# Kernel tuning notes

Measured on AMD Instinct MI355X. Metric: run time of the kernel, lower is better.

## Reference

```python
import jax, jax.numpy as jnp
import numpy as np

N_QUBITS = 12
N_LAYERS = 2
PATCH = 16
NPS = 14  # patches per side for 224/16
N_PATCHES = NPS * NPS
SCALE = 1.0 / np.sqrt(N_QUBITS)


def _butterfly_gates(n):
    # Faithful replication of QuantumOrthogonalLayer.butterfly_circuit indexing:
    # param_idx increments even when the (idx1, idx2) pair is skipped.
    gates, pidx = [], 0
    n_bl = int(np.ceil(np.log2(n)))
    for layer in range(n_bl):
        stride = 2 ** layer
        for start in range(0, n - stride, 2 * stride):
            for off in range(stride):
                i1, i2 = start + off, start + off + stride
                if i1 < n and i2 < n:
                    gates.append((pidx, i1, i2))
                pidx += 1
    nppl = sum(2 ** (n_bl - 1 - i) * 2 ** i for i in range(n_bl))  # n_params() = 32
    return gates, nppl

GATES, NPPL = _butterfly_gates(N_QUBITS)

# Pauli-Z sign table: qubit 0 is the most-significant bit of the flattened state index.
_bits = (np.arange(2 ** N_QUBITS)[:, None] >> np.arange(N_QUBITS - 1, -1, -1)[None, :]) & 1
Z_SIGNS = jnp.asarray(1.0 - 2.0 * _bits, dtype=jnp.float32)  # (4096, 12)


def _rbs_u(theta):
    # 4x4 real unitary of RY(2t,w1); CNOT(w1,w2); RY(-2t,w1); CNOT(w1,w2)
    c, s = jnp.cos(theta), jnp.sin(theta)
    c2, s2, cs = c * c, s * s, c * s
    return jnp.stack([
        jnp.stack([c2, s2, -cs, cs]),
        jnp.stack([s2, c2, cs, -cs]),
        jnp.stack([cs, -cs, c2, s2]),
        jnp.stack([-cs, cs, s2, c2]),
    ])


def _apply_2q(state, U, i, j):
    # state: (P, 2, 2, ..., 2); apply U to qubit axes i, j
    st = jnp.moveaxis(state, (1 + i, 1 + j), (-2, -1))
    shp = st.shape
    st = st.reshape(shp[:-2] + (4,)) @ U.T
    return jnp.moveaxis(st.reshape(shp), (-2, -1), (1 + i, 1 + j))


@jax.checkpoint
def quantum_expvals(features, params):
    # features: (P, n_qubits) angles; params: (N_LAYERS * NPPL,)
    P = features.shape[0]
    half = 0.5 * features
    amp = jnp.stack([jnp.cos(half), jnp.sin(half)], axis=-1)  # (P, n, 2) RY(x)|0>
    state = jnp.ones((P, 1), features.dtype)
    for q in range(N_QUBITS):  # product-state angle encoding
        state = (state[:, :, None] * amp[:, q][:, None, :]).reshape(P, -1)
    state = state.reshape((P,) + (2,) * N_QUBITS)
    for l in range(N_LAYERS):
        base = l * NPPL
        for pidx, w1, w2 in GATES:
            state = _apply_2q(state, _rbs_u(params[base + pidx]), w1, w2)
    probs = state.reshape(P, -1) ** 2
    return probs @ Z_SIGNS  # (P, n_qubits) <Z_i>


def setup_inputs() -> dict:
    key = jax.random.key(0)
    ks = jax.random.split(key, 6)
    x = jax.random.normal(ks[0], (4, 3, 224, 224), dtype=jnp.float32)
    W_proj = jax.random.normal(ks[1], (N_QUBITS, PATCH * PATCH), dtype=jnp.float32) / np.sqrt(PATCH * PATCH)
    b_proj = jnp.zeros((N_QUBITS,), jnp.float32)
    q_params = 0.1 * jax.random.normal(ks[2], (N_LAYERS * NPPL,), dtype=jnp.float32)
    k_params = 0.1 * jax.random.normal(ks[3], (N_LAYERS * NPPL,), dtype=jnp.float32)
    v_params = 0.1 * jax.random.normal(ks[4], (N_LAYERS * NPPL,), dtype=jnp.float32)
    W_cls = jax.random.normal(ks[5], (1000, N_PATCHES * N_QUBITS), dtype=jnp.float32) / np.sqrt(N_PATCHES * N_QUBITS)
    b_cls = jnp.zeros((1000,), jnp.float32)
    return {"x": x, "W_proj": W_proj, "b_proj": b_proj, "q_params": q_params,
            "k_params": k_params, "v_params": v_params, "W_cls": W_cls, "b_cls": b_cls}


def reference(x, W_proj, b_proj, q_params, k_params, v_params, W_cls, b_cls):
    B = x.shape[0]
    xg = jnp.mean(x, axis=1)  # channel average -> (B, H, W)
    patches = xg.reshape(B, NPS, PATCH, NPS, PATCH).transpose(0, 1, 3, 2, 4)
    patches = patches.reshape(B, N_PATCHES, PATCH * PATCH)
    proj = patches @ W_proj.T + b_proj  # (B, n_patches, n_qubits)
    feats = proj.reshape(-1, N_QUBITS)
    Q = quantum_expvals(feats, q_params).reshape(B, N_PATCHES, N_QUBITS)
    K = quantum_expvals(feats, k_params).reshape(B, N_PATCHES, N_QUBITS)
    V = quantum_expvals(feats, v_params).reshape(B, N_PATCHES, N_QUBITS)
    attn = jax.nn.softmax(jnp.einsum('bqd,bkd->bqk', Q, K) * SCALE, axis=-1)
    out = jnp.einsum('bqk,bkd->bqd', attn, V)  # (B, n_patches, n_qubits)
    logits = out.reshape(B, -1) @ W_cls.T + b_cls
    return logits
```

## Files before the change

### kernel.cpp

```cpp
#include <hip/hip_runtime.h>
#include <math.h>

#define NQ        12
#define NPS       14
#define NPATCH    196
#define NB        4
#define NCLS      1000
#define FEATDIM   2352
#define SCALE_F   0.28867513459481287f

typedef float v2f __attribute__((ext_vector_type(2)));

constexpr int PRa[8][5] = {
    {2,3,0,1, 4},
    {2,3,4,5, 6},
    {2,3,5,6, 7},
    {2,3,0,4, 6},
    {2,3,8,9,10},
    {2,3,9,10,11},
    {2,3,0,8,10},
    {2,3,1,5, 9},
};
constexpr int PTa[8][7] = {
    {5,6,7,8,9,10,11},
    {7,0,1,8,9,10,11},
    {0,1,4,8,9,10,11},
    {8,9,10,1,5,7,11},
    {4,0,1,5,6,7,11},
    {0,1,8,5,6,7,4},
    {1,5,9,6,7,11,4},
    {6,0,11,7,8,10,4},
};
constexpr bool BARa[8] = {false,false,false,false,true,false,false,true};

constexpr int STRIDE = 20;

constexpr int cwgt2(int X, int q) {
    for (int k = 0; k < 4; ++k) if (PRa[X][k] == q) return 1 << k;
    if (PRa[X][4] == q) return 0;
    for (int m = 0; m < 7; ++m) if (PTa[X][m] == q) return STRIDE << m;
    return 0;
}
constexpr int rimm2(int X, int Y, int a) {
    int s = 0;
    for (int j = 0; j < 3; ++j)
        if ((a >> j) & 1) s += cwgt2(X, PRa[Y][2 + j]);
    return s;
}
constexpr int splitpos(int X) {
    int Y = (X + 1) & 7, H = PRa[X][4];
    for (int j = 0; j < 3; ++j) if (PRa[Y][2 + j] == H) return j;
    for (int m = 0; m < 7; ++m) if (PTa[Y][m] == H) return 8 + m;
    return -1;
}

template<int TI>
__device__ __forceinline__ void relayout2(v2f amp2[16], float* lds, int tid, int base) {
    constexpr int X = TI, Y = (TI + 1) & 7;
    constexpr int SP = splitpos(TI);
    constexpr bool BAR = BARa[TI];
    float4* dst = (float4*)(lds + STRIDE * tid);

    #pragma unroll
    for (int k = 0; k < 4; ++k)
        dst[k] = make_float4(amp2[2*k][0], amp2[2*k][1], amp2[2*k+1][0], amp2[2*k+1][1]);
    if (BAR) __syncthreads();

    float4 rvh[4];

    if constexpr (SP < 3) {
        #pragma unroll
        for (int a = 0; a < 8; ++a) {
            if ((a >> SP) & 1) continue;
            float4 v = *(const float4*)(lds + base + rimm2(X, Y, a));
            if (a < 4) {
                amp2[2*a][0]   = v.x; amp2[2*a][1]   = v.y;
                amp2[2*a+1][0] = v.z; amp2[2*a+1][1] = v.w;
            } else {
                rvh[a-4] = v;
            }
        }
        if (BAR) __syncthreads();
        #pragma unroll
        for (int k = 0; k < 4; ++k)
            dst[k] = make_float4(amp2[8+2*k][0], amp2[8+2*k][1], amp2[9+2*k][0], amp2[9+2*k][1]);
        #pragma unroll
        for (int a = 4; a < 8; ++a) {
            if ((a >> SP) & 1) continue;
            amp2[2*a][0]   = rvh[a-4].x; amp2[2*a][1]   = rvh[a-4].y;
            amp2[2*a+1][0] = rvh[a-4].z; amp2[2*a+1][1] = rvh[a-4].w;
        }
        if (BAR) __syncthreads();
        #pragma unroll
        for (int a = 0; a < 8; ++a) {
            if (!((a >> SP) & 1)) continue;
            float4 v = *(const float4*)(lds + base + rimm2(X, Y, a));
            amp2[2*a][0]   = v.x; amp2[2*a][1]   = v.y;
            amp2[2*a+1][0] = v.z; amp2[2*a+1][1] = v.w;
        }
        if (BAR) __syncthreads();
    } else {
        constexpr int TB = SP - 8;
        const bool p0 = ((tid >> TB) & 1) == 0;
        if (p0) {
            #pragma unroll
            for (int a = 0; a < 4; ++a) {
                float4 v = *(const float4*)(lds + base + rimm2(X, Y, a));
                amp2[2*a][0]   = v.x; amp2[2*a][1]   = v.y;
                amp2[2*a+1][0] = v.z; amp2[2*a+1][1] = v.w;
            }
            #pragma unroll
            for (int a = 4; a < 8; ++a)
                rvh[a-4] = *(const float4*)(lds + base + rimm2(X, Y, a));
        }
        if (BAR) __syncthreads();
        #pragma unroll
        for (int k = 0; k < 4; ++k)
            dst[k] = make_float4(amp2[8+2*k][0], amp2[8+2*k][1], amp2[9+2*k][0], amp2[9+2*k][1]);
        if (BAR) __syncthreads();
        if (p0) {
            #pragma unroll
            for (int a = 4; a < 8; ++a) {
                amp2[2*a][0]   = rvh[a-4].x; amp2[2*a][1]   = rvh[a-4].y;
                amp2[2*a+1][0] = rvh[a-4].z; amp2[2*a+1][1] = rvh[a-4].w;
            }
        } else {
            #pragma unroll
            for (int a = 0; a < 8; ++a) {
                float4 v = *(const float4*)(lds + base + rimm2(X, Y, a));
                amp2[2*a][0]   = v.x; amp2[2*a][1]   = v.y;
                amp2[2*a+1][0] = v.z; amp2[2*a+1][1] = v.w;
            }
        }
        if (BAR) __syncthreads();
    }
}

template<int MI, int MJ>
__device__ __forceinline__ void pk_gate(v2f a[16], float gc, float gs) {
    v2f H = {0.5f, 0.5f}, C = {gc, gc}, S = {gs, gs};
    #pragma unroll
    for (int m = 0; m < 16; ++m) {
        if (m & (MI | MJ)) continue;
        v2f a0 = a[m], a1 = a[m | MJ], a2 = a[m | MI], a3 = a[m | MI | MJ];
        v2f p  = a0 + a1, q  = a0 - a1;
        v2f p2 = a2 + a3, q2 = a2 - a3;
        v2f t1 = H * p  + C * q  - S * q2;
        v2f t2 = H * p2 + C * q2 + S * q;
        a[m]           = t1;
        a[m | MJ]      = p  - t1;
        a[m | MI]      = t2;
        a[m | MI | MJ] = p2 - t2;
    }
}

template<int MI, int MJ>
__device__ __forceinline__ void sc_gate(float* amp, float gc, float gs) {
    #pragma unroll
    for (int m = 0; m < 32; ++m) {
        if (m & (MI | MJ)) continue;
        float a0 = amp[m], a1 = amp[m | MJ], a2 = amp[m | MI], a3 = amp[m | MI | MJ];
        float p  = a0 + a1, q  = a0 - a1;
        float p2 = a2 + a3, q2 = a2 - a3;
        float t1 = 0.5f * p  + gc * q  - gs * q2;
        float t2 = 0.5f * p2 + gc * q2 + gs * q;
        amp[m]           = t1;
        amp[m | MJ]      = p  - t1;
        amp[m | MI]      = t2;
        amp[m | MI | MJ] = p2 - t2;
    }
}

template<int CTRL>
__device__ __forceinline__ float dppadd(float x) {
    int s = __builtin_amdgcn_update_dpp(0, __float_as_int(x), CTRL, 0xf, 0xf, true);
    return x + __int_as_float(s);
}
__device__ __forceinline__ float wave_sum(float x) {
    x = dppadd<0x111>(x);
    x = dppadd<0x112>(x);
    x = dppadd<0x114>(x);
    x = dppadd<0x118>(x);
    x = dppadd<0x142>(x);
    x = dppadd<0x143>(x);
    return x;
}

__global__ __launch_bounds__(128, 5) void qcirc_kernel(
    const float* __restrict__ x,
    const float* __restrict__ Wp,
    const float* __restrict__ bproj,
    const float* __restrict__ qp,
    const float* __restrict__ kp,
    const float* __restrict__ vp,
    float* __restrict__ qkv)
{
    __shared__ __align__(16) float lds[STRIDE * 128];
    __shared__ float chs[NQ], shs[NQ];
    __shared__ float gC[40], gS[40];
    __shared__ float red2[2][12];

    const int tid = threadIdx.x;
    const int p = blockIdx.x, b = blockIdx.y, c = blockIdx.z;
    const int bp = b * NPATCH + p;
    const float* params = (c == 0) ? qp : (c == 1) ? kp : vp;
    const int lane = tid & 63, wv = tid >> 6;

    float part[NQ];
    #pragma unroll
    for (int q = 0; q < NQ; ++q) part[q] = 0.0f;
    {
        int py = p / NPS, px = p % NPS;
        const float* xb = x + (size_t)b * 3 * 224 * 224;
        #pragma unroll
        for (int k = 0; k < 2; ++k) {
            int pix = tid + 128 * k;
            int off = (py * 16 + (pix >> 4)) * 224 + px * 16 + (pix & 15);
            float v = (xb[off] + xb[off + 50176] + xb[off + 100352]) * (1.0f / 3.0f);
            #pragma unroll
            for (int q = 0; q < NQ; ++q) part[q] += v * Wp[q * 256 + pix];
        }
    }
    if (tid < 40) {
        int l = tid / 20, g = tid - l * 20;
        float th = params[l * 32 + g];
        gC[tid] = 0.5f * cosf(2.0f * th);
        gS[tid] = 0.5f * sinf(2.0f * th);
    }
    #pragma unroll
    for (int q = 0; q < NQ; ++q) part[q] = wave_sum(part[q]);
    if (lane == 63) {
        #pragma unroll
        for (int q = 0; q < NQ; ++q) red2[wv][q] = part[q];
    }
    __syncthreads();
    if (tid < NQ) {
        float h = 0.5f * (red2[0][tid] + red2[1][tid] + bproj[tid]);
        chs[tid] = cosf(h); shs[tid] = sinf(h);
    }
    __syncthreads();

    int baseT[8];
    #pragma unroll
    for (int TI = 0; TI < 8; ++TI) {
        int Y = (TI + 1) & 7, s = 0;
        #pragma unroll
        for (int j = 0; j < 7; ++j)
            s += ((tid >> j) & 1) ? cwgt2(TI, PTa[Y][j]) : 0;
        baseT[TI] = s;
    }

    v2f amp2[16];
    float* amp = (float*)amp2;
    {
        float hi = ((tid &  1) ? shs[5]  : chs[5])  *
                   ((tid &  2) ? shs[6]  : chs[6])  *
                   ((tid &  4) ? shs[7]  : chs[7])  *
                   ((tid &  8) ? shs[8]  : chs[8])  *
                   ((tid & 16) ? shs[9]  : chs[9])  *
                   ((tid & 32) ? shs[10] : chs[10]) *
                   ((tid & 64) ? shs[11] : chs[11]);
        float pA[8], pB[4];
        #pragma unroll
        for (int i = 0; i < 8; ++i)
            pA[i] = ((i & 1) ? shs[2] : chs[2]) * ((i & 2) ? shs[3] : chs[3]) *
                    ((i & 4) ? shs[0] : chs[0]);
        #pragma unroll
        for (int i = 0; i < 4; ++i)
            pB[i] = ((i & 1) ? shs[1] : chs[1]) * ((i & 2) ? shs[4] : chs[4]);
        #pragma unroll
        for (int r = 0; r < 32; ++r) amp[r] = pA[r & 7] * pB[r >> 3] * hi;
    }

    #pragma unroll 1
    for (int l = 0; l < 2; ++l) {
        const int bb = l * 20;
        pk_gate<2, 4>(amp2, gC[bb+0], gS[bb+0]);
        sc_gate<1, 2>(amp,  gC[bb+1], gS[bb+1]);
        sc_gate<4, 1>(amp,  gC[bb+6], gS[bb+6]);
        pk_gate<4, 1>(amp2, gC[bb+7], gS[bb+7]);
        relayout2<0>(amp2, lds, tid, baseT[0]);
        pk_gate<2, 4>(amp2, gC[bb+2], gS[bb+2]);
        relayout2<1>(amp2, lds, tid, baseT[1]);
        pk_gate<4, 8>(amp2, gC[bb+3],  gS[bb+3]);
        pk_gate<2, 8>(amp2, gC[bb+9],  gS[bb+9]);
        pk_gate<1, 8>(amp2, gC[bb+15], gS[bb+15]);
        relayout2<2>(amp2, lds, tid, baseT[2]);
        pk_gate<4, 8>(amp2, gC[bb+8],  gS[bb+8]);
        pk_gate<2, 4>(amp2, gC[bb+12], gS[bb+12]);
        sc_gate<1,16>(amp,  gC[bb+14], gS[bb+14]);
        relayout2<3>(amp2, lds, tid, baseT[3]);
        pk_gate<2, 4>(amp2, gC[bb+4], gS[bb+4]);
        relayout2<4>(amp2, lds, tid, baseT[4]);
        pk_gate<4, 8>(amp2, gC[bb+5],  gS[bb+5]);
        pk_gate<2, 8>(amp2, gC[bb+11], gS[bb+11]);
        pk_gate<1, 8>(amp2, gC[bb+19], gS[bb+19]);
        relayout2<5>(amp2, lds, tid, baseT[5]);
        pk_gate<4, 8>(amp2, gC[bb+10], gS[bb+10]);
        pk_gate<2, 4>(amp2, gC[bb+16], gS[bb+16]);
        sc_gate<1,16>(amp,  gC[bb+18], gS[bb+18]);
        relayout2<6>(amp2, lds, tid, baseT[6]);
        pk_gate<2, 4>(amp2, gC[bb+13], gS[bb+13]);
        pk_gate<2, 8>(amp2, gC[bb+17], gS[bb+17]);
        if (l == 0) relayout2<7>(amp2, lds, tid, baseT[7]);
    }

    float T, Sq2, Sq3, Sq1, Sq5, Sq9;
    {
        float t1[16]; Sq2 = 0.0f;
        #pragma unroll
        for (int i = 0; i < 16; ++i) {
            float e = amp[2*i] * amp[2*i], o = amp[2*i+1] * amp[2*i+1];
            t1[i] = e + o; Sq2 += e - o;
        }
        float t2[8]; Sq3 = 0.0f;
        #pragma unroll
        for (int i = 0; i < 8; ++i) { t2[i] = t1[2*i] + t1[2*i+1]; Sq3 += t1[2*i] - t1[2*i+1]; }
        float t3[4]; Sq1 = 0.0f;
        #pragma unroll
        for (int i = 0; i < 4; ++i) { t3[i] = t2[2*i] + t2[2*i+1]; Sq1 += t2[2*i] - t2[2*i+1]; }
        float t4[2]; Sq5 = 0.0f;
        #pragma unroll
        for (int i = 0; i < 2; ++i) { t4[i] = t3[2*i] + t3[2*i+1]; Sq5 += t3[2*i] - t3[2*i+1]; }
        T = t4[0] + t4[1]; Sq9 = t4[0] - t4[1];
    }
    float Vq6  = (tid &  1) ? -T : T;
    float Vq0  = (tid &  2) ? -T : T;
    float Vq11 = (tid &  4) ? -T : T;
    float Vq7  = (tid &  8) ? -T : T;
    float Vq8  = (tid & 16) ? -T : T;
    float Vq10 = (tid & 32) ? -T : T;
    T    = wave_sum(T);
    Vq6  = wave_sum(Vq6);  Vq0  = wave_sum(Vq0);  Vq11 = wave_sum(Vq11);
    Vq7  = wave_sum(Vq7);  Vq8  = wave_sum(Vq8);  Vq10 = wave_sum(Vq10);
    Sq2  = wave_sum(Sq2);  Sq3  = wave_sum(Sq3);  Sq1  = wave_sum(Sq1);
    Sq5  = wave_sum(Sq5);  Sq9  = wave_sum(Sq9);
    if (lane == 63) {
        red2[wv][0]  = Vq0;  red2[wv][1]  = Sq1;  red2[wv][2]  = Sq2;
        red2[wv][3]  = Sq3;  red2[wv][4]  = T;    red2[wv][5]  = Sq5;
        red2[wv][6]  = Vq6;  red2[wv][7]  = Vq7;  red2[wv][8]  = Vq8;
        red2[wv][9]  = Sq9;  red2[wv][10] = Vq10; red2[wv][11] = Vq11;
    }
    __syncthreads();
    if (tid < NQ) {
        float v1 = red2[1][tid];
        float s = red2[0][tid] + ((tid == 4) ? -v1 : v1);
        qkv[((size_t)c * (NB * NPATCH) + bp) * NQ + tid] = s;
    }
}

__global__ __launch_bounds__(256) void attn_kernel(
    const float* __restrict__ qkv,
    float* __restrict__ outb)
{
    int tid = threadIdx.x;
    int qp = blockIdx.x, b = blockIdx.y;
    const float* Q = qkv;
    const float* K = qkv + NB * NPATCH * NQ;
    const float* V = qkv + 2 * NB * NPATCH * NQ;

    __shared__ float redm[4], reds[4], redv[4][NQ];

    float4 q0 = ((const float4*)(Q + (b * NPATCH + qp) * NQ))[0];
    float4 q1 = ((const float4*)(Q + (b * NPATCH + qp) * NQ))[1];
    float4 q2 = ((const float4*)(Q + (b * NPATCH + qp) * NQ))[2];

    float score = -1e30f;
    float4 v0, v1, v2;
    if (tid < NPATCH) {
        const float4* K4 = (const float4*)(K + (b * NPATCH + tid) * NQ);
        float4 k0 = K4[0], k1 = K4[1], k2 = K4[2];
        float s = q0.x*k0.x + q0.y*k0.y + q0.z*k0.z + q0.w*k0.w
                + q1.x*k1.x + q1.y*k1.y + q1.z*k1.z + q1.w*k1.w
                + q2.x*k2.x + q2.y*k2.y + q2.z*k2.z + q2.w*k2.w;
        score = s * SCALE_F;
        const float4* V4 = (const float4*)(V + (b * NPATCH + tid) * NQ);
        v0 = V4[0]; v1 = V4[1]; v2 = V4[2];
    }
    float m = score;
    #pragma unroll
    for (int o = 32; o > 0; o >>= 1) m = fmaxf(m, __shfl_down(m, o));
    int lane = tid & 63, wv = tid >> 6;
    if (lane == 0) redm[wv] = m;
    __syncthreads();
    float maxv = fmaxf(fmaxf(redm[0], redm[1]), fmaxf(redm[2], redm[3]));

    float w = (tid < NPATCH) ? expf(score - maxv) : 0.0f;
    float sm = w;
    #pragma unroll
    for (int o = 32; o > 0; o >>= 1) sm += __shfl_down(sm, o);
    if (lane == 0) reds[wv] = sm;

    float part[NQ];
    #pragma unroll
    for (int d = 0; d < NQ; d++) part[d] = 0.0f;
    if (tid < NPATCH) {
        part[0] = w*v0.x; part[1] = w*v0.y; part[2]  = w*v0.z; part[3]  = w*v0.w;
        part[4] = w*v1.x; part[5] = w*v1.y; part[6]  = w*v1.z; part[7]  = w*v1.w;
        part[8] = w*v2.x; part[9] = w*v2.y; part[10] = w*v2.z; part[11] = w*v2.w;
    }
    #pragma unroll
    for (int d = 0; d < NQ; d++) {
        #pragma unroll
        for (int o = 32; o > 0; o >>= 1) part[d] += __shfl_down(part[d], o);
    }
    if (lane == 0) {
        #pragma unroll
        for (int d = 0; d < NQ; d++) redv[wv][d] = part[d];
    }
    __syncthreads();
    if (tid < NQ) {
        float sumv = reds[0] + reds[1] + reds[2] + reds[3];
        float s = redv[0][tid] + redv[1][tid] + redv[2][tid] + redv[3][tid];
        outb[(size_t)b * FEATDIM + qp * NQ + tid] = s / sumv;
    }
}

__global__ __launch_bounds__(256) void cls_kernel(
    const float* __restrict__ outb,
    const float* __restrict__ Wc,
    const float* __restrict__ bc,
    float* __restrict__ logits)
{
    int o = blockIdx.x, tid = threadIdx.x;
    float acc[NB] = {0.0f, 0.0f, 0.0f, 0.0f};
    const float4* w4 = (const float4*)(Wc + (size_t)o * FEATDIM);
    for (int j = tid; j < FEATDIM / 4; j += 256) {
        float4 w = w4[j];
        #pragma unroll
        for (int b = 0; b < NB; b++) {
            float4 ov = ((const float4*)(outb + (size_t)b * FEATDIM))[j];
            acc[b] += w.x*ov.x + w.y*ov.y + w.z*ov.z + w.w*ov.w;
        }
    }
    #pragma unroll
    for (int b = 0; b < NB; b++) {
        #pragma unroll
        for (int off = 32; off > 0; off >>= 1) acc[b] += __shfl_down(acc[b], off);
    }
    __shared__ float red[4][NB];
    int lane = tid & 63, wv = tid >> 6;
    if (lane == 0) {
        #pragma unroll
        for (int b = 0; b < NB; b++) red[wv][b] = acc[b];
    }
    __syncthreads();
    if (tid < NB) {
        float s = red[0][tid] + red[1][tid] + red[2][tid] + red[3][tid];
        logits[(size_t)tid * NCLS + o] = s + bc[o];
    }
}

extern "C" void kernel_launch(void* const* d_in, const int* in_sizes, int n_in,
                              void* d_out, int out_size, void* d_ws, size_t ws_size,
                              hipStream_t stream) {
    const float* x     = (const float*)d_in[0];
    const float* Wp    = (const float*)d_in[1];
    const float* bproj = (const float*)d_in[2];
    const float* qp    = (const float*)d_in[3];
    const float* kp    = (const float*)d_in[4];
    const float* vp    = (const float*)d_in[5];
    const float* Wc    = (const float*)d_in[6];
    const float* bc    = (const float*)d_in[7];
    float* logits = (float*)d_out;

    float* ws   = (float*)d_ws;
    float* qkv  = ws;
    float* outb = ws + 28224;

    qcirc_kernel<<<dim3(NPATCH, NB, 3), 128, 0, stream>>>(x, Wp, bproj, qp, kp, vp, qkv);
    attn_kernel <<<dim3(NPATCH, NB),    256, 0, stream>>>(qkv, outb);
    cls_kernel  <<<NCLS,                256, 0, stream>>>(outb, Wc, bc, logits);
}
```

Measured before the change: 118.5 us.

## Fuse attention and classifier kernels with global counter barrier; pack scalar gates

Merges the attention and classifier launches into one kernel. The first 784 blocks compute attention rows and bump a global atomic counter, and all 1000 blocks spin on that counter before running the classifier GEMV. This removes one kernel launch and its gap. Intermediates move from the workspace into device globals, and qcirc block 0 sets the target counter value. Separately, the scalar sc_gate paths are replaced with packed v2f gates that use lane swizzles, so the whole state stays in packed form. The spin barrier depends on every attention block being resident or finishing before the waiting blocks occupy all slots, which risks deadlock or stall under contention.

```diff
diff --git a/kernel.cpp b/kernel.cpp
--- a/kernel.cpp
+++ b/kernel.cpp
@@ -10,6 +10,11 @@
 #define SCALE_F   0.28867513459481287f
 
 typedef float v2f __attribute__((ext_vector_type(2)));
+
+__device__ float    g_qkv[3 * NB * NPATCH * NQ];
+__device__ float    g_outb[NB * FEATDIM];
+__device__ unsigned g_sync;
+__device__ unsigned g_target;
 
 constexpr int PRa[8][5] = {
     {2,3,0,1, 4},
@@ -154,20 +159,34 @@
     }
 }
 
-template<int MI, int MJ>
-__device__ __forceinline__ void sc_gate(float* amp, float gc, float gs) {
-    #pragma unroll
-    for (int m = 0; m < 32; ++m) {
-        if (m & (MI | MJ)) continue;
-        float a0 = amp[m], a1 = amp[m | MJ], a2 = amp[m | MI], a3 = amp[m | MI | MJ];
-        float p  = a0 + a1, q  = a0 - a1;
-        float p2 = a2 + a3, q2 = a2 - a3;
-        float t1 = 0.5f * p  + gc * q  - gs * q2;
-        float t2 = 0.5f * p2 + gc * q2 + gs * q;
-        amp[m]           = t1;
-        amp[m | MJ]      = p  - t1;
-        amp[m | MI]      = t2;
-        amp[m | MI | MJ] = p2 - t2;
+template<int MJ2>
+__device__ __forceinline__ void pq1_gate(v2f a[16], float gc, float gs) {
+    v2f H = {0.5f, 0.5f}, C = {gc, gc}, S2 = {-gs, gs};
+    #pragma unroll
+    for (int i = 0; i < 16; ++i) {
+        if (i & MJ2) continue;
+        v2f A = a[i], B = a[i | MJ2];
+        v2f P = A + B, Q = A - B;
+        v2f Qs = __builtin_shufflevector(Q, Q, 1, 0);
+        v2f T = H * P + C * Q + S2 * Qs;
+        a[i]       = T;
+        a[i | MJ2] = P - T;
+    }
+}
+
+template<int MI2>
+__device__ __forceinline__ void pq6_gate(v2f a[16], float gc, float gs) {
+    v2f H = {0.5f, 0.5f}, C = {gc, gc}, Sp = {gs, gs}, Sn = {-gs, -gs};
+    #pragma unroll
+    for (int i = 0; i < 16; ++i) {
+        if (i & MI2) continue;
+        v2f A = a[i], D = a[i | MI2];
+        v2f As = __builtin_shufflevector(A, A, 1, 0);
+        v2f Ds = __builtin_shufflevector(D, D, 1, 0);
+        v2f X  = A + As, Y  = A - As;
+        v2f X2 = D + Ds, Y2 = D - Ds;
+        a[i]       = H * X  + C * Y  + Sn * Y2;
+        a[i | MI2] = H * X2 + C * Y2 + Sp * Y;
     }
 }
 
@@ -192,8 +211,7 @@
     const float* __restrict__ bproj,
     const float* __restrict__ qp,
     const float* __restrict__ kp,
-    const float* __restrict__ vp,
-    float* __restrict__ qkv)
+    const float* __restrict__ vp)
 {
     __shared__ __align__(16) float lds[STRIDE * 128];
     __shared__ float chs[NQ], shs[NQ];
@@ -205,6 +223,10 @@
     const int bp = b * NPATCH + p;
     const float* params = (c == 0) ? qp : (c == 1) ? kp : vp;
     const int lane = tid & 63, wv = tid >> 6;
+
+    if (p == 0 && b == 0 && c == 0 && tid == 0)
+        g_target = __hip_atomic_load(&g_sync, __ATOMIC_RELAXED,
+                                     __HIP_MEMORY_SCOPE_AGENT) + (unsigned)NB * NPATCH;
 
     float part[NQ];
     #pragma unroll
@@ -276,8 +298,8 @@
     for (int l = 0; l < 2; ++l) {
         const int bb = l * 20;
         pk_gate<2, 4>(amp2, gC[bb+0], gS[bb+0]);
-        sc_gate<1, 2>(amp,  gC[bb+1], gS[bb+1]);
-        sc_gate<4, 1>(amp,  gC[bb+6], gS[bb+6]);
+        pq1_gate<1>(amp2,   gC[bb+1], gS[bb+1]);
+        pq6_gate<2>(amp2,   gC[bb+6], gS[bb+6]);
         pk_gate<4, 1>(amp2, gC[bb+7], gS[bb+7]);
         relayout2<0>(amp2, lds, tid, baseT[0]);
         pk_gate<2, 4>(amp2, gC[bb+2], gS[bb+2]);
@@ -288,7 +310,7 @@
         relayout2<2>(amp2, lds, tid, baseT[2]);
         pk_gate<4, 8>(amp2, gC[bb+8],  gS[bb+8]);
         pk_gate<2, 4>(amp2, gC[bb+12], gS[bb+12]);
-        sc_gate<1,16>(amp,  gC[bb+14], gS[bb+14]);
+        pq1_gate<8>(amp2,   gC[bb+14], gS[bb+14]);
         relayout2<3>(amp2, lds, tid, baseT[3]);
         pk_gate<2, 4>(amp2, gC[bb+4], gS[bb+4]);
         relayout2<4>(amp2, lds, tid, baseT[4]);
@@ -298,7 +320,7 @@
         relayout2<5>(amp2, lds, tid, baseT[5]);
         pk_gate<4, 8>(amp2, gC[bb+10], gS[bb+10]);
         pk_gate<2, 4>(amp2, gC[bb+16], gS[bb+16]);
-        sc_gate<1,16>(amp,  gC[bb+18], gS[bb+18]);
+        pq1_gate<8>(amp2,   gC[bb+18], gS[bb+18]);
         relayout2<6>(amp2, lds, tid, baseT[6]);
         pk_gate<2, 4>(amp2, gC[bb+13], gS[bb+13]);
         pk_gate<2, 8>(amp2, gC[bb+17], gS[bb+17]);
@@ -345,91 +367,103 @@
     if (tid < NQ) {
         float v1 = red2[1][tid];
         float s = red2[0][tid] + ((tid == 4) ? -v1 : v1);
-        qkv[((size_t)c * (NB * NPATCH) + bp) * NQ + tid] = s;
-    }
-}
-
-__global__ __launch_bounds__(256) void attn_kernel(
-    const float* __restrict__ qkv,
-    float* __restrict__ outb)
-{
-    int tid = threadIdx.x;
-    int qp = blockIdx.x, b = blockIdx.y;
-    const float* Q = qkv;
-    const float* K = qkv + NB * NPATCH * NQ;
-    const float* V = qkv + 2 * NB * NPATCH * NQ;
-
-    __shared__ float redm[4], reds[4], redv[4][NQ];
-
-    float4 q0 = ((const float4*)(Q + (b * NPATCH + qp) * NQ))[0];
-    float4 q1 = ((const float4*)(Q + (b * NPATCH + qp) * NQ))[1];
-    float4 q2 = ((const float4*)(Q + (b * NPATCH + qp) * NQ))[2];
-
-    float score = -1e30f;
-    float4 v0, v1, v2;
-    if (tid < NPATCH) {
-        const float4* K4 = (const float4*)(K + (b * NPATCH + tid) * NQ);
-        float4 k0 = K4[0], k1 = K4[1], k2 = K4[2];
-        float s = q0.x*k0.x + q0.y*k0.y + q0.z*k0.z + q0.w*k0.w
-                + q1.x*k1.x + q1.y*k1.y + q1.z*k1.z + q1.w*k1.w
-                + q2.x*k2.x + q2.y*k2.y + q2.z*k2.z + q2.w*k2.w;
-        score = s * SCALE_F;
-        const float4* V4 = (const float4*)(V + (b * NPATCH + tid) * NQ);
-        v0 = V4[0]; v1 = V4[1]; v2 = V4[2];
-    }
-    float m = score;
-    #pragma unroll
-    for (int o = 32; o > 0; o >>= 1) m = fmaxf(m, __shfl_down(m, o));
-    int lane = tid & 63, wv = tid >> 6;
-    if (lane == 0) redm[wv] = m;
-    __syncthreads();
-    float maxv = fmaxf(fmaxf(redm[0], redm[1]), fmaxf(redm[2], redm[3]));
-
-    float w = (tid < NPATCH) ? expf(score - maxv) : 0.0f;
-    float sm = w;
-    #pragma unroll
-    for (int o = 32; o > 0; o >>= 1) sm += __shfl_down(sm, o);
-    if (lane == 0) reds[wv] = sm;
-
-    float part[NQ];
-    #pragma unroll
-    for (int d = 0; d < NQ; d++) part[d] = 0.0f;
-    if (tid < NPATCH) {
-        part[0] = w*v0.x; part[1] = w*v0.y; part[2]  = w*v0.z; part[3]  = w*v0.w;
-        part[4] = w*v1.x; part[5] = w*v1.y; part[6]  = w*v1.z; part[7]  = w*v1.w;
-        part[8] = w*v2.x; part[9] = w*v2.y; part[10] = w*v2.z; part[11] = w*v2.w;
-    }
-    #pragma unroll
-    for (int d = 0; d < NQ; d++) {
-        #pragma unroll
-        for (int o = 32; o > 0; o >>= 1) part[d] += __shfl_down(part[d], o);
-    }
-    if (lane == 0) {
-        #pragma unroll
-        for (int d = 0; d < NQ; d++) redv[wv][d] = part[d];
-    }
-    __syncthreads();
-    if (tid < NQ) {
-        float sumv = reds[0] + reds[1] + reds[2] + reds[3];
-        float s = redv[0][tid] + redv[1][tid] + redv[2][tid] + redv[3][tid];
-        outb[(size_t)b * FEATDIM + qp * NQ + tid] = s / sumv;
-    }
-}
-
-__global__ __launch_bounds__(256) void cls_kernel(
-    const float* __restrict__ outb,
+        g_qkv[((size_t)c * (NB * NPATCH) + bp) * NQ + tid] = s;
+    }
+}
+
+__global__ __launch_bounds__(256) void attncls_kernel(
     const float* __restrict__ Wc,
     const float* __restrict__ bc,
     float* __restrict__ logits)
 {
-    int o = blockIdx.x, tid = threadIdx.x;
+    int bid = blockIdx.x, tid = threadIdx.x;
+    int lane = tid & 63, wv = tid >> 6;
+    const float* Q = g_qkv;
+    const float* K = g_qkv + NB * NPATCH * NQ;
+    const float* V = g_qkv + 2 * NB * NPATCH * NQ;
+
+    __shared__ float redm[4], reds[4], redv[4][NQ];
+
+    if (bid < NB * NPATCH) {
+        int b = bid / NPATCH, qp = bid - b * NPATCH;
+
+        float4 q0 = ((const float4*)(Q + (b * NPATCH + qp) * NQ))[0];
+        float4 q1 = ((const float4*)(Q + (b * NPATCH + qp) * NQ))[1];
+        float4 q2 = ((const float4*)(Q + (b * NPATCH + qp) * NQ))[2];
+
+        float score = -1e30f;
+        float4 v0, v1, v2;
+        if (tid < NPATCH) {
+            const float4* K4 = (const float4*)(K + (b * NPATCH + tid) * NQ);
+            float4 k0 = K4[0], k1 = K4[1], k2 = K4[2];
+            float s = q0.x*k0.x + q0.y*k0.y + q0.z*k0.z + q0.w*k0.w
+                    + q1.x*k1.x + q1.y*k1.y + q1.z*k1.z + q1.w*k1.w
+                    + q2.x*k2.x + q2.y*k2.y + q2.z*k2.z + q2.w*k2.w;
+            score = s * SCALE_F;
+            const float4* V4 = (const float4*)(V + (b * NPATCH + tid) * NQ);
+            v0 = V4[0]; v1 = V4[1]; v2 = V4[2];
+        }
+        float m = score;
+        #pragma unroll
+        for (int o = 32; o > 0; o >>= 1) m = fmaxf(m, __shfl_down(m, o));
+        if (lane == 0) redm[wv] = m;
+        __syncthreads();
+        float maxv = fmaxf(fmaxf(redm[0], redm[1]), fmaxf(redm[2], redm[3]));
+
+        float w = (tid < NPATCH) ? expf(score - maxv) : 0.0f;
+        float sm = w;
+        #pragma unroll
+        for (int o = 32; o > 0; o >>= 1) sm += __shfl_down(sm, o);
+        if (lane == 0) reds[wv] = sm;
+
+        float part[NQ];
+        #pragma unroll
+        for (int d = 0; d < NQ; d++) part[d] = 0.0f;
+        if (tid < NPATCH) {
+            part[0] = w*v0.x; part[1] = w*v0.y; part[2]  = w*v0.z; part[3]  = w*v0.w;
+            part[4] = w*v1.x; part[5] = w*v1.y; part[6]  = w*v1.z; part[7]  = w*v1.w;
+            part[8] = w*v2.x; part[9] = w*v2.y; part[10] = w*v2.z; part[11] = w*v2.w;
+        }
+        #pragma unroll
+        for (int d = 0; d < NQ; d++) {
+            #pragma unroll
+            for (int o = 32; o > 0; o >>= 1) part[d] += __shfl_down(part[d], o);
+        }
+        if (lane == 0) {
+            #pragma unroll
+            for (int d = 0; d < NQ; d++) redv[wv][d] = part[d];
+        }
+        __syncthreads();
+        if (tid < NQ) {
+            float sumv = reds[0] + reds[1] + reds[2] + reds[3];
+            float s = redv[0][tid] + redv[1][tid] + redv[2][tid] + redv[3][tid];
+            g_outb[(size_t)b * FEATDIM + qp * NQ + tid] = s / sumv;
+        }
+        __syncthreads();
+        if (tid == 0) {
+            __threadfence();
+            __hip_atomic_fetch_add(&g_sync, 1u, __ATOMIC_RELEASE,
+                                   __HIP_MEMORY_SCOPE_AGENT);
+        }
+    }
+
+    if (tid == 0) {
+        unsigned tgt = g_target;
+        while ((int)(tgt - __hip_atomic_load(&g_sync, __ATOMIC_ACQUIRE,
+                                             __HIP_MEMORY_SCOPE_AGENT)) > 0)
+            __builtin_amdgcn_s_sleep(32);
+    }
+    __syncthreads();
+    __threadfence();
+
+    int o = bid;
     float acc[NB] = {0.0f, 0.0f, 0.0f, 0.0f};
     const float4* w4 = (const float4*)(Wc + (size_t)o * FEATDIM);
     for (int j = tid; j < FEATDIM / 4; j += 256) {
         float4 w = w4[j];
         #pragma unroll
         for (int b = 0; b < NB; b++) {
-            float4 ov = ((const float4*)(outb + (size_t)b * FEATDIM))[j];
+            float4 ov = ((const float4*)(g_outb + (size_t)b * FEATDIM))[j];
             acc[b] += w.x*ov.x + w.y*ov.y + w.z*ov.z + w.w*ov.w;
         }
     }
@@ -439,7 +473,6 @@
         for (int off = 32; off > 0; off >>= 1) acc[b] += __shfl_down(acc[b], off);
     }
     __shared__ float red[4][NB];
-    int lane = tid & 63, wv = tid >> 6;
     if (lane == 0) {
         #pragma unroll
         for (int b = 0; b < NB; b++) red[wv][b] = acc[b];
@@ -463,12 +496,8 @@
     const float* Wc    = (const float*)d_in[6];
     const float* bc    = (const float*)d_in[7];
     float* logits = (float*)d_out;
-
-    float* ws   = (float*)d_ws;
-    float* qkv  = ws;
-    float* outb = ws + 28224;
-
-    qcirc_kernel<<<dim3(NPATCH, NB, 3), 128, 0, stream>>>(x, Wp, bproj, qp, kp, vp, qkv);
-    attn_kernel <<<dim3(NPATCH, NB),    256, 0, stream>>>(qkv, outb);
-    cls_kernel  <<<NCLS,                256, 0, stream>>>(outb, Wc, bc, logits);
-}
+    (void)d_ws; (void)ws_size;
+
+    qcirc_kernel  <<<dim3(NPATCH, NB, 3), 128, 0, stream>>>(x, Wp, bproj, qp, kp, vp);
+    attncls_kernel<<<NCLS,                256, 0, stream>>>(Wc, bc, logits);
+}
```

After: 249.2 us. 110% more time.
